# Kernel optimization log

Measured on AMD Instinct MI355X. Metric: run time of the kernel, lower is better.

## Reference

```python
import jax, jax.numpy as jnp
import numpy as np
import math

THETA = 10000.0

def _rope(x, pos):
    # x: [B, H, S, Dh], pos: [S]
    d = x.shape[-1]
    inv_freq = 1.0 / (THETA ** (jnp.arange(0, d, 2, dtype=jnp.float32) / d))  # [Dh/2]
    ang = pos.astype(jnp.float32)[:, None] * inv_freq[None, :]                # [S, Dh/2]
    cos, sin = jnp.cos(ang), jnp.sin(ang)
    x1, x2 = x[..., 0::2], x[..., 1::2]
    r1 = x1 * cos - x2 * sin
    r2 = x1 * sin + x2 * cos
    return jnp.stack([r1, r2], axis=-1).reshape(x.shape)

def setup_inputs() -> dict:
    key = jax.random.key(0)
    ks = jax.random.split(key, 5)
    B, S, D = 2, 1024, 2048
    Dkv = 512
    scale = 1.0 / math.sqrt(D)
    return {
        "X": jax.random.normal(ks[0], (B, S, D), dtype=jnp.float32),
        "token_positions": jnp.arange(S, dtype=jnp.int32),
        "q_w": jax.random.normal(ks[1], (D, D), dtype=jnp.float32) * scale,
        "k_w": jax.random.normal(ks[2], (Dkv, D), dtype=jnp.float32) * scale,
        "v_w": jax.random.normal(ks[3], (Dkv, D), dtype=jnp.float32) * scale,
        "o_w": jax.random.normal(ks[4], (D, D), dtype=jnp.float32) * scale,
    }

def reference(X, token_positions, q_w, k_w, v_w, o_w):
    B, S, D = X.shape
    H, Hkv = 32, 8
    Dh = D // H
    G = H // Hkv  # query heads per KV head

    Q = (X @ q_w.T).reshape(B, S, H, Dh).transpose(0, 2, 1, 3)      # [B,H,S,Dh]
    K = (X @ k_w.T).reshape(B, S, Hkv, Dh).transpose(0, 2, 1, 3)    # [B,Hkv,S,Dh]
    V = (X @ v_w.T).reshape(B, S, Hkv, Dh).transpose(0, 2, 1, 3)    # [B,Hkv,S,Dh]

    Q = _rope(Q, token_positions)
    K = _rope(K, token_positions)

    # group query heads: [B, Hkv, G, S, Dh]
    Qg = Q.reshape(B, Hkv, G, S, Dh)
    scores = jnp.einsum('bkgqd,bkld->bkgql', Qg, K) / math.sqrt(Dh)  # [B,Hkv,G,S,S]
    causal = jnp.tril(jnp.ones((S, S), dtype=bool))
    scores = jnp.where(causal, scores, -jnp.inf)
    probs = jax.nn.softmax(scores, axis=-1)
    attn = jnp.einsum('bkgql,bkld->bkgqd', probs, V)                 # [B,Hkv,G,S,Dh]

    attn = attn.reshape(B, H, S, Dh).transpose(0, 2, 1, 3).reshape(B, S, D)
    return attn @ o_w.T
```

## Files before the change

### kernel.cpp

```cpp
#include <hip/hip_runtime.h>

typedef _Float16 f16;
typedef _Float16 half8 __attribute__((ext_vector_type(8), may_alias));
typedef _Float16 half4 __attribute__((ext_vector_type(4), may_alias));
typedef float f32x4 __attribute__((ext_vector_type(4), may_alias));

#define ROPE_KF -0.41524101186092027f

__device__ __forceinline__ void gload_lds16(const f16* g, f16* lds) {
  __builtin_amdgcn_global_load_lds(
      (const __attribute__((address_space(1))) void*)g,
      (__attribute__((address_space(3))) void*)lds, 16, 0, 0);
}

template <int N>
__device__ __forceinline__ void vm_wait() {
  if constexpr (N == 0) asm volatile("s_waitcnt vmcnt(0)" ::: "memory");
  else if constexpr (N == 3) asm volatile("s_waitcnt vmcnt(3)" ::: "memory");
  else if constexpr (N == 4) asm volatile("s_waitcnt vmcnt(4)" ::: "memory");
  else if constexpr (N == 6) asm volatile("s_waitcnt vmcnt(6)" ::: "memory");
  else if constexpr (N == 8) asm volatile("s_waitcnt vmcnt(8)" ::: "memory");
}

__device__ __forceinline__ half8 rope8(half8 v, float posf, int i0, float scale) {
  half8 r;
#pragma unroll
  for (int p = 0; p < 4; ++p) {
    const float ang = posf * exp2f(ROPE_KF * (float)(i0 + p));
    float s, c;
    sincosf(ang, &s, &c);
    const float x1 = (float)v[2 * p], x2 = (float)v[2 * p + 1];
    r[2 * p]     = (f16)((x1 * c - x2 * s) * scale);
    r[2 * p + 1] = (f16)((x1 * s + x2 * c) * scale);
  }
  return r;
}

__global__ __launch_bounds__(256) void cvt_all(const float* __restrict__ s0, f16* __restrict__ d0, int n0,
                                               const float* __restrict__ s1, f16* __restrict__ d1, int n1,
                                               const float* __restrict__ s2, f16* __restrict__ d2, int n2,
                                               const float* __restrict__ s3, f16* __restrict__ d3, int n3,
                                               const float* __restrict__ s4, f16* __restrict__ d4, int n4) {
  const int step = gridDim.x * blockDim.x * 4;
  const int base = (blockIdx.x * blockDim.x + threadIdx.x) * 4;
  auto go = [&](const float* s, f16* d, int n) {
    for (int i = base; i < n; i += step) {
      float4 v = *(const float4*)(s + i);
      half4 h;
      h[0] = (f16)v.x; h[1] = (f16)v.y; h[2] = (f16)v.z; h[3] = (f16)v.w;
      *(half4*)(d + i) = h;
    }
  };
  go(s0, d0, n0); go(s1, d1, n1); go(s2, d2, n2); go(s3, d3, n3); go(s4, d4, n4);
}

template <int OUT_F32, int BM>
__global__ __launch_bounds__(256, 2) void gemm_bt(const f16* __restrict__ A,
                                                  const f16* __restrict__ B,
                                                  void* __restrict__ Cv,
                                                  int M, int N, int K) {
  constexpr int NJ = (BM == 128) ? 4 : 2;
  constexpr int ACH = BM / 64;
  constexpr int LPS = ACH + 2;

  __shared__ alignas(16) f16 As[4][BM][32];
  __shared__ alignas(16) f16 Bs[4][128][32];
  const int tid = threadIdx.x;
  const int w = tid >> 6, l = tid & 63;
  const int m0 = blockIdx.y * BM, n0 = blockIdx.x << 7;
  const int fr = l & 15;
  const int fkz = (((l >> 4) ^ ((fr >> 1) & 3)) << 3);
  const int wr = (BM == 128) ? ((w >> 1) << 6) : 0;
  const int wc = (BM == 128) ? ((w & 1) << 6) : (w << 5);
  const int srow = l >> 2;
  const int scol = (((l & 3) ^ ((l >> 3) & 3)) << 3);

  const f16* ga = A + (size_t)(m0 + srow) * K + scol;
  const f16* gb = B + (size_t)(n0 + srow) * K + scol;

  auto stage = [&](int t) {
    const int buf = t & 3, k0 = t << 5;
#pragma unroll
    for (int c = 0; c < ACH; ++c) {
      const int rb = (w * ACH + c) << 4;
      gload_lds16(ga + (size_t)rb * K + k0, &As[buf][rb][0]);
    }
#pragma unroll
    for (int c = 0; c < 2; ++c) {
      const int rb = (w * 2 + c) << 4;
      gload_lds16(gb + (size_t)rb * K + k0, &Bs[buf][rb][0]);
    }
  };

  half8 afA[4], bfA[NJ], afB[4], bfB[NJ];
  auto readfrags = [&](int t, half8* af, half8* bf) {
    const int buf = t & 3;
#pragma unroll
    for (int i = 0; i < 4; ++i) af[i] = *(const half8*)&As[buf][wr + i * 16 + fr][fkz];
#pragma unroll
    for (int j = 0; j < NJ; ++j) bf[j] = *(const half8*)&Bs[buf][wc + j * 16 + fr][fkz];
  };

  f32x4 acc[4][NJ] = {};
  auto mm = [&](half8* af, half8* bf) {
#pragma unroll
    for (int i = 0; i < 4; ++i)
#pragma unroll
      for (int j = 0; j < NJ; ++j)
        acc[i][j] = __builtin_amdgcn_mfma_f32_16x16x32_f16(af[i], bf[j], acc[i][j], 0, 0, 0);
  };

  const int nk = K >> 5;
  stage(0); stage(1); stage(2);
  vm_wait<2 * LPS>();
  __builtin_amdgcn_s_barrier();
  __builtin_amdgcn_sched_barrier(0);
  readfrags(0, afA, bfA);

  for (int t = 0; t < nk; t += 2) {
    if (t + 2 < nk) vm_wait<LPS>(); else vm_wait<0>();
    __builtin_amdgcn_s_barrier();
    __builtin_amdgcn_sched_barrier(0);
    if (t + 3 < nk) stage(t + 3);
    if (t + 1 < nk) readfrags(t + 1, afB, bfB);
    mm(afA, bfA);
    __builtin_amdgcn_sched_barrier(0);
    if (t + 1 < nk) {
      if (t + 3 < nk) vm_wait<LPS>(); else vm_wait<0>();
      __builtin_amdgcn_s_barrier();
      __builtin_amdgcn_sched_barrier(0);
      if (t + 4 < nk) stage(t + 4);
      if (t + 2 < nk) readfrags(t + 2, afA, bfA);
      mm(afB, bfB);
      __builtin_amdgcn_sched_barrier(0);
    }
  }

  const int orow = (l >> 4) << 2;
#pragma unroll
  for (int i = 0; i < 4; ++i) {
#pragma unroll
    for (int j = 0; j < NJ; ++j) {
      const int col = n0 + wc + j * 16 + fr;
#pragma unroll
      for (int r = 0; r < 4; ++r) {
        const size_t idx = (size_t)(m0 + wr + i * 16 + orow + r) * N + col;
        if (OUT_F32) ((float*)Cv)[idx] = acc[i][j][r];
        else ((f16*)Cv)[idx] = (f16)acc[i][j][r];
      }
    }
  }
}

__global__ __launch_bounds__(256) void repack_kv(const f16* __restrict__ QKV,
                                                 const int* __restrict__ pos,
                                                 f16* __restrict__ Kp,
                                                 f16* __restrict__ Vt) {
  const int kt = blockIdx.x, kvh = blockIdx.y, b = blockIdx.z;
  const int tid = threadIdx.x;
  __shared__ f16 vs[64][72];
  const size_t tile = ((size_t)((b * 8 + kvh) * 16 + kt)) * 4096;
  const f16* kbase = QKV + 2048 + kvh * 64;
  const f16* vbase = QKV + 2560 + kvh * 64;
#pragma unroll
  for (int p = 0; p < 2; ++p) {
    const int c = tid + p * 256;
    const int row = c >> 3, slot = c & 7;
    const size_t grow = (size_t)(b * 1024 + kt * 64 + row) * 3072;
    half8 kk = *(const half8*)(kbase + grow + slot * 8);
    kk = rope8(kk, (float)pos[kt * 64 + row], slot << 2, 1.0f);
    *(half8*)(Kp + tile + row * 64 + ((slot ^ (row & 7)) << 3)) = kk;
    *(half8*)&vs[row][slot * 8] = *(const half8*)(vbase + grow + slot * 8);
  }
  __syncthreads();
#pragma unroll
  for (int p = 0; p < 2; ++p) {
    const int c = tid + p * 256;
    const int d = c >> 3, oct = c & 7;
    half8 vv;
#pragma unroll
    for (int m = 0; m < 8; ++m) vv[m] = vs[oct * 8 + m][d];
    *(half8*)(Vt + tile + d * 64 + ((oct ^ (d & 7)) << 3)) = vv;
  }
}

__global__ __launch_bounds__(256) void attn_fwd(const f16* __restrict__ QKV,
                                                const f16* __restrict__ Kp,
                                                const f16* __restrict__ Vt,
                                                const int* __restrict__ pos,
                                                f16* __restrict__ O) {
  const int flat = blockIdx.x + (blockIdx.y << 3) + (blockIdx.z << 8);
  const int rmid = ((flat & 7) << 6) + (flat >> 3);
  const int pr = rmid & 7, h = (rmid >> 3) & 31, b = rmid >> 8;
  const int kvh = h >> 2;
  const int tid = threadIdx.x, w = tid >> 6, l = tid & 63;
  const int fr = l & 15, g = l >> 4;
  const int orow = g << 2;
  const int qtA = pr, qtB = 15 - pr;

  __shared__ alignas(16) char KsB[2][8192];
  __shared__ alignas(16) char VtB[2][8192];
  __shared__ alignas(16) f16 Ps[4][16][72];

  auto KS = [&](int buf, int row, int slot) -> f16* {
    return (f16*)(KsB[buf] + row * 128 + ((slot ^ (row & 7)) << 4));
  };
  auto VT = [&](int buf, int d, int oct) -> f16* {
    return (f16*)(VtB[buf] + d * 128 + ((oct ^ (d & 7)) << 4));
  };

  const int sA = qtA * 64 + w * 16 + fr, sB = qtB * 64 + w * 16 + fr;
  const float pA = (float)pos[sA], pB = (float)pos[sB];
  const size_t qoff = (size_t)(b * 1024 + w * 16 + fr) * 3072 + h * 64 + (g << 3);
  const f16* qA = QKV + qoff + (size_t)qtA * 64 * 3072;
  const f16* qB = QKV + qoff + (size_t)qtB * 64 * 3072;
  const half8 aA0 = rope8(*(const half8*)qA, pA, g << 2, 0.125f);
  const half8 aA1 = rope8(*(const half8*)(qA + 32), pA, 16 + (g << 2), 0.125f);
  const half8 aB0 = rope8(*(const half8*)qB, pB, g << 2, 0.125f);
  const half8 aB1 = rope8(*(const half8*)(qB + 32), pB, 16 + (g << 2), 0.125f);

  float rmA[4], rlA[4], rmB[4], rlB[4];
  f32x4 oA[4] = {}, oB[4] = {};
#pragma unroll
  for (int r = 0; r < 4; ++r) { rmA[r] = rmB[r] = -3.0e38f; rlA[r] = rlB[r] = 0.f; }

  const size_t tbase = ((size_t)((b * 8 + kvh) * 16)) * 4096;
  const f16* kp0 = Kp + tbase + w * 1024 + (l << 3);
  const f16* vp0 = Vt + tbase + w * 1024 + (l << 3);
  auto stage = [&](int buf, int kt) {
    const f16* kp = kp0 + (size_t)kt * 4096;
    const f16* vp = vp0 + (size_t)kt * 4096;
    f16* kl = (f16*)(KsB[buf] + w * 2048);
    f16* vl = (f16*)(VtB[buf] + w * 2048);
    gload_lds16(kp, kl);
    gload_lds16(kp + 512, kl + 512);
    gload_lds16(vp, vl);
    gload_lds16(vp + 512, vl + 512);
  };

  auto compute = [&](int buf, const half8& a0, const half8& a1, float* rm, float* rl,
                     f32x4* o, int qt, int kt) {
    f32x4 s4[4] = {};
#pragma unroll
    for (int j = 0; j < 4; ++j) {
      const half8 bk0 = *(const half8*)KS(buf, j * 16 + fr, g);
      const half8 bk1 = *(const half8*)KS(buf, j * 16 + fr, 4 + g);
      s4[j] = __builtin_amdgcn_mfma_f32_16x16x32_f16(a0, bk0, s4[j], 0, 0, 0);
      s4[j] = __builtin_amdgcn_mfma_f32_16x16x32_f16(a1, bk1, s4[j], 0, 0, 0);
    }
    if (kt == qt) {
      const int qrow0 = qt * 64 + w * 16 + orow;
#pragma unroll
      for (int j = 0; j < 4; ++j) {
        const int col = kt * 64 + j * 16 + fr;
#pragma unroll
        for (int r = 0; r < 4; ++r)
          if (col > qrow0 + r) s4[j][r] = -1.0e30f;
      }
    }
#pragma unroll
    for (int r = 0; r < 4; ++r) {
      float mx = fmaxf(fmaxf(s4[0][r], s4[1][r]), fmaxf(s4[2][r], s4[3][r]));
#pragma unroll
      for (int off = 8; off >= 1; off >>= 1) mx = fmaxf(mx, __shfl_xor(mx, off));
      const float mn = fmaxf(rm[r], mx);
      const float sf = __expf(rm[r] - mn);
      rl[r] *= sf;
      o[0][r] *= sf; o[1][r] *= sf; o[2][r] *= sf; o[3][r] *= sf;
      rm[r] = mn;
    }
    float ps[4] = {0.f, 0.f, 0.f, 0.f};
#pragma unroll
    for (int j = 0; j < 4; ++j)
#pragma unroll
      for (int r = 0; r < 4; ++r) {
        const float p = __expf(s4[j][r] - rm[r]);
        ps[r] += p;
        Ps[w][orow + r][j * 16 + fr] = (f16)p;
      }
#pragma unroll
    for (int r = 0; r < 4; ++r) {
      float t = ps[r];
#pragma unroll
      for (int off = 8; off >= 1; off >>= 1) t += __shfl_xor(t, off);
      rl[r] += t;
    }
#pragma unroll
    for (int kv2 = 0; kv2 < 2; ++kv2) {
      const half8 ap = *(const half8*)&Ps[w][fr][kv2 * 32 + (g << 3)];
#pragma unroll
      for (int j = 0; j < 4; ++j) {
        const half8 bv = *(const half8*)VT(buf, j * 16 + fr, kv2 * 4 + g);
        o[j] = __builtin_amdgcn_mfma_f32_16x16x32_f16(ap, bv, o[j], 0, 0, 0);
      }
    }
  };

  stage(0, 0);
  stage(1, 1);
  for (int kt = 0; kt <= qtB; ++kt) {
    const int buf = kt & 1;
    if (kt < qtB) vm_wait<4>();
    else vm_wait<0>();
    __builtin_amdgcn_s_barrier();
    __builtin_amdgcn_sched_barrier(0);
    if (kt <= qtA) compute(buf, aA0, aA1, rmA, rlA, oA, qtA, kt);
    compute(buf, aB0, aB1, rmB, rlB, oB, qtB, kt);
    __builtin_amdgcn_sched_barrier(0);
    __builtin_amdgcn_s_barrier();
    if (kt + 2 <= qtB) stage(buf, kt + 2);
  }

#pragma unroll
  for (int j = 0; j < 4; ++j)
#pragma unroll
    for (int r = 0; r < 4; ++r) {
      const int rowA = qtA * 64 + w * 16 + orow + r;
      const int rowB = qtB * 64 + w * 16 + orow + r;
      const int col = h * 64 + j * 16 + fr;
      O[(size_t)(b * 1024 + rowA) * 2048 + col] = (f16)(oA[j][r] / rlA[r]);
      O[(size_t)(b * 1024 + rowB) * 2048 + col] = (f16)(oB[j][r] / rlB[r]);
    }
}

extern "C" void kernel_launch(void* const* d_in, const int* in_sizes, int n_in,
                              void* d_out, int out_size, void* d_ws, size_t ws_size,
                              hipStream_t stream) {
  const float* X = (const float*)d_in[0];
  const int* tokpos = (const int*)d_in[1];
  const float* qw = (const float*)d_in[2];
  const float* kw = (const float*)d_in[3];
  const float* vw = (const float*)d_in[4];
  const float* ow = (const float*)d_in[5];

  constexpr int B = 2, S = 1024, D = 2048, DKV = 512, H = 32;
  constexpr int M = B * S;
  constexpr int NQKV = D + 2 * DKV;

  char* ws = (char*)d_ws;
  f16* Xh   = (f16*)(ws);
  f16* QKVW = (f16*)(ws + (8u << 20));
  f16* owh  = (f16*)(ws + (20u << 20));
  f16* QKVc = (f16*)(ws + (28u << 20));
  f16* Ah   = (f16*)(ws + (40u << 20));
  f16* Kp   = (f16*)(ws);
  f16* Vt   = (f16*)(ws + (2u << 20));

  cvt_all<<<2048, 256, 0, stream>>>(X, Xh, M * D,
                                    qw, QKVW, D * D,
                                    kw, QKVW + (size_t)D * D, DKV * D,
                                    vw, QKVW + (size_t)(D + DKV) * D, DKV * D,
                                    ow, owh, D * D);

  gemm_bt<0, 128><<<dim3(NQKV / 128, M / 128), 256, 0, stream>>>(Xh, QKVW, QKVc, M, NQKV, D);

  repack_kv<<<dim3(16, 8, 2), 256, 0, stream>>>(QKVc, tokpos, Kp, Vt);

  attn_fwd<<<dim3(8, H, B), 256, 0, stream>>>(QKVc, Kp, Vt, tokpos, Ah);

  gemm_bt<1, 64><<<dim3(D / 128, M / 64), 256, 0, stream>>>(Ah, owh, d_out, M, D, D);
}
```

Measured before the change: 142.7 us.

## Triple-buffer attention K/V, simplify GEMM pipeline, add MFMA priority hints

The GEMM main loop drops its manual two-stage register double-buffering of fragments. It now reads fragments and issues MFMAs in the same iteration, with s_setprio raised around the MFMA block. The attention kernel moves from two to three LDS buffers for K/V, which lets it issue the next stage right after the barrier and drop the second barrier per iteration. The cost is more LDS per block, which may lower occupancy, and fragment reads in the GEMM that are no longer overlapped with the previous tile's MFMAs.

```diff
diff --git a/kernel.cpp b/kernel.cpp
--- a/kernel.cpp
+++ b/kernel.cpp
@@ -92,48 +92,31 @@
     }
   };
 
-  half8 afA[4], bfA[NJ], afB[4], bfB[NJ];
-  auto readfrags = [&](int t, half8* af, half8* bf) {
-    const int buf = t & 3;
-#pragma unroll
-    for (int i = 0; i < 4; ++i) af[i] = *(const half8*)&As[buf][wr + i * 16 + fr][fkz];
-#pragma unroll
-    for (int j = 0; j < NJ; ++j) bf[j] = *(const half8*)&Bs[buf][wc + j * 16 + fr][fkz];
-  };
-
   f32x4 acc[4][NJ] = {};
-  auto mm = [&](half8* af, half8* bf) {
-#pragma unroll
-    for (int i = 0; i < 4; ++i)
-#pragma unroll
-      for (int j = 0; j < NJ; ++j)
-        acc[i][j] = __builtin_amdgcn_mfma_f32_16x16x32_f16(af[i], bf[j], acc[i][j], 0, 0, 0);
-  };
 
   const int nk = K >> 5;
   stage(0); stage(1); stage(2);
-  vm_wait<2 * LPS>();
-  __builtin_amdgcn_s_barrier();
-  __builtin_amdgcn_sched_barrier(0);
-  readfrags(0, afA, bfA);
-
-  for (int t = 0; t < nk; t += 2) {
-    if (t + 2 < nk) vm_wait<LPS>(); else vm_wait<0>();
+  for (int t = 0; t < nk; ++t) {
+    if (t + 2 < nk) vm_wait<2 * LPS>();
+    else if (t + 1 < nk) vm_wait<LPS>();
+    else vm_wait<0>();
     __builtin_amdgcn_s_barrier();
     __builtin_amdgcn_sched_barrier(0);
     if (t + 3 < nk) stage(t + 3);
-    if (t + 1 < nk) readfrags(t + 1, afB, bfB);
-    mm(afA, bfA);
+    const int buf = t & 3;
+    half8 af[4], bf[NJ];
+#pragma unroll
+    for (int i = 0; i < 4; ++i) af[i] = *(const half8*)&As[buf][wr + i * 16 + fr][fkz];
+#pragma unroll
+    for (int j = 0; j < NJ; ++j) bf[j] = *(const half8*)&Bs[buf][wc + j * 16 + fr][fkz];
+    __builtin_amdgcn_s_setprio(1);
+#pragma unroll
+    for (int i = 0; i < 4; ++i)
+#pragma unroll
+      for (int j = 0; j < NJ; ++j)
+        acc[i][j] = __builtin_amdgcn_mfma_f32_16x16x32_f16(af[i], bf[j], acc[i][j], 0, 0, 0);
+    __builtin_amdgcn_s_setprio(0);
     __builtin_amdgcn_sched_barrier(0);
-    if (t + 1 < nk) {
-      if (t + 3 < nk) vm_wait<LPS>(); else vm_wait<0>();
-      __builtin_amdgcn_s_barrier();
-      __builtin_amdgcn_sched_barrier(0);
-      if (t + 4 < nk) stage(t + 4);
-      if (t + 2 < nk) readfrags(t + 2, afA, bfA);
-      mm(afB, bfB);
-      __builtin_amdgcn_sched_barrier(0);
-    }
   }
 
   const int orow = (l >> 4) << 2;
@@ -198,8 +181,8 @@
   const int orow = g << 2;
   const int qtA = pr, qtB = 15 - pr;
 
-  __shared__ alignas(16) char KsB[2][8192];
-  __shared__ alignas(16) char VtB[2][8192];
+  __shared__ alignas(16) char KsB[3][8192];
+  __shared__ alignas(16) char VtB[3][8192];
   __shared__ alignas(16) f16 Ps[4][16][72];
 
   auto KS = [&](int buf, int row, int slot) -> f16* {
@@ -227,7 +210,8 @@
   const size_t tbase = ((size_t)((b * 8 + kvh) * 16)) * 4096;
   const f16* kp0 = Kp + tbase + w * 1024 + (l << 3);
   const f16* vp0 = Vt + tbase + w * 1024 + (l << 3);
-  auto stage = [&](int buf, int kt) {
+  auto stage = [&](int kt) {
+    const int buf = kt % 3;
     const f16* kp = kp0 + (size_t)kt * 4096;
     const f16* vp = vp0 + (size_t)kt * 4096;
     f16* kl = (f16*)(KsB[buf] + w * 2048);
@@ -241,6 +225,7 @@
   auto compute = [&](int buf, const half8& a0, const half8& a1, float* rm, float* rl,
                      f32x4* o, int qt, int kt) {
     f32x4 s4[4] = {};
+    __builtin_amdgcn_s_setprio(1);
 #pragma unroll
     for (int j = 0; j < 4; ++j) {
       const half8 bk0 = *(const half8*)KS(buf, j * 16 + fr, g);
@@ -248,6 +233,7 @@
       s4[j] = __builtin_amdgcn_mfma_f32_16x16x32_f16(a0, bk0, s4[j], 0, 0, 0);
       s4[j] = __builtin_amdgcn_mfma_f32_16x16x32_f16(a1, bk1, s4[j], 0, 0, 0);
     }
+    __builtin_amdgcn_s_setprio(0);
     if (kt == qt) {
       const int qrow0 = qt * 64 + w * 16 + orow;
 #pragma unroll
@@ -285,6 +271,7 @@
       for (int off = 8; off >= 1; off >>= 1) t += __shfl_xor(t, off);
       rl[r] += t;
     }
+    __builtin_amdgcn_s_setprio(1);
 #pragma unroll
     for (int kv2 = 0; kv2 < 2; ++kv2) {
       const half8 ap = *(const half8*)&Ps[w][fr][kv2 * 32 + (g << 3)];
@@ -294,21 +281,21 @@
         o[j] = __builtin_amdgcn_mfma_f32_16x16x32_f16(ap, bv, o[j], 0, 0, 0);
       }
     }
-  };
-
-  stage(0, 0);
-  stage(1, 1);
+    __builtin_amdgcn_s_setprio(0);
+  };
+
+  stage(0);
+  stage(1);
   for (int kt = 0; kt <= qtB; ++kt) {
-    const int buf = kt & 1;
     if (kt < qtB) vm_wait<4>();
     else vm_wait<0>();
     __builtin_amdgcn_s_barrier();
     __builtin_amdgcn_sched_barrier(0);
+    if (kt + 2 <= qtB) stage(kt + 2);
+    const int buf = kt % 3;
     if (kt <= qtA) compute(buf, aA0, aA1, rmA, rlA, oA, qtA, kt);
     compute(buf, aB0, aB1, rmB, rlB, oB, qtB, kt);
     __builtin_amdgcn_sched_barrier(0);
-    __builtin_amdgcn_s_barrier();
-    if (kt + 2 <= qtB) stage(buf, kt + 2);
   }
 
 #pragma unroll
```

Measured after the change: 142.1 us. About the same (-0.4%).
